# Optimization experiments

Measured on AMD Instinct MI355X. Metric: run time of the kernel, lower is better.

## Reference

```python
import jax, jax.numpy as jnp
import numpy as np
import math

L, N, D = 1024, 64, 64
O = 1024

def setup_inputs() -> dict:
    key = jax.random.key(0)
    k1, k2 = jax.random.split(key)
    x = jax.random.normal(k1, (L, N, D), dtype=jnp.float32)
    upfold = jax.random.normal(k2, (O, N, D), dtype=jnp.float32)
    return {"x": x, "upfold": upfold}

def reference(x, upfold):
    # x: [L, N, D], upfold: [O, N, D]
    d = x.shape[-1]
    scale = 1.0 / math.sqrt(d)
    # affinities: [L, O, N]
    affinities = jnp.einsum('lnd,ond->lon', x, upfold) * scale
    # weighted sum with (sigmoid - 0.5) weights: [L, N, D]
    features = jnp.einsum('lon,ond->lnd', jax.nn.sigmoid(affinities) - 0.5, upfold)
    return features
```

## Files before the change

### kernel.cpp

```cpp
#include <hip/hip_runtime.h>
#include <stdint.h>

#define L_DIM 1024
#define N_DIM 64
#define D_DIM 64
#define O_DIM 1024
#define ND    4096
#define NT    8

typedef float    floatx16 __attribute__((ext_vector_type(16)));
typedef _Float16 half8    __attribute__((ext_vector_type(8)));
typedef _Float16 h2       __attribute__((ext_vector_type(2)));
typedef __fp16   fp16x2   __attribute__((ext_vector_type(2)));

__device__ __forceinline__ uint32_t pkh2(float a, float b) {
    fp16x2 p = __builtin_amdgcn_cvt_pkrtz(a, b);
    return __builtin_bit_cast(uint32_t, p);
}

__device__ __forceinline__ half8 mk_frag(uint32_t a, uint32_t b, uint32_t c, uint32_t d) {
    union { uint32_t u[4]; half8 v; } U;
    U.u[0] = a; U.u[1] = b; U.u[2] = c; U.u[3] = d;
    return U.v;
}

__device__ __forceinline__ uint32_t psig(float s0, float s1) {
    const h2 HI = {(_Float16)41.6f,        (_Float16)41.6f};
    const h2 LO = {(_Float16)-41.6f,       (_Float16)-41.6f};
    const h2 SC = {(_Float16)0.0625f,      (_Float16)0.0625f};
    const h2 C0 = {(_Float16)0.03099238f,  (_Float16)0.03099238f};
    const h2 C1 = {(_Float16)-0.00842090f, (_Float16)-0.00842090f};
    const h2 C2 = {(_Float16)0.00151845f,  (_Float16)0.00151845f};
    const h2 C3 = {(_Float16)-1.02197e-4f, (_Float16)-1.02197e-4f};
    h2 s = __builtin_bit_cast(h2, pkh2(s0, s1));
    s = __builtin_elementwise_min(s, HI);
    s = __builtin_elementwise_max(s, LO);
    h2 ha = s * SC;
    h2 v  = ha * ha;
    h2 w  = C2 + v * C3;
    w     = C1 + v * w;
    w     = C0 + v * w;
    h2 f  = s * w;
    return __builtin_bit_cast(uint32_t, f);
}

__device__ __forceinline__ void load_tile(const float* ubase, int team, int ot,
                                          int g, int c, float4* va, float4* vb) {
    const float* pr = ubase + (size_t)(team * 512 + ot * 64 + 2 * g) * ND + 4 * c;
    #pragma unroll
    for (int j = 0; j < 4; ++j) {
        va[j] = *(const float4*)(pr + (size_t)(16 * j) * ND);
        vb[j] = *(const float4*)(pr + (size_t)(16 * j) * ND + ND);
    }
}

__global__ void __launch_bounds__(256, 4)
corr_kernel(const float* __restrict__ x, const float* __restrict__ up,
            float* __restrict__ out)
{
    __shared__ __align__(16) unsigned char smem[36864];
    uint16_t (*Ub)[64][72]  = (uint16_t (*)[64][72])smem;
    uint32_t (*Ut2)[32][68] = (uint32_t (*)[32][68])(smem + 18432);
    float    (*Fred)[2][2][32][16] = (float (*)[2][2][32][16])smem;
    float    (*Xs)[68] = (float (*)[68])smem;

    const int tid  = threadIdx.x;
    const int lane = tid & 63;
    const int wid  = tid >> 6;
    const int l31  = lane & 31;
    const int h    = lane >> 5;
    const int team = wid >> 1;
    const int wrow = wid & 1;
    const int ttid = tid & 127;
    const int c    = ttid & 15;
    const int g    = ttid >> 4;
    const int n    = blockIdx.x;
    const int lb   = blockIdx.y;
    const int lw   = lb * 64 + wrow * 32 + l31;

    const float* ubase = up + (size_t)n * D_DIM;

    float4 va[4], vb[4];
    load_tile(ubase, team, 0, g, c, va, vb);

    half8 Xf[4];
    {
        const int xr = tid >> 2;
        const int xc = tid & 3;
        const float* xsrc = x + (size_t)(lb * 64 + xr) * ND + n * D_DIM;
        #pragma unroll
        for (int j = 0; j < 4; ++j) {
            float4 f = *(const float4*)(xsrc + 4 * (xc + 4 * j));
            *(float4*)&Xs[xr][4 * (xc + 4 * j)] = f;
        }
        __syncthreads();
        const int rl = wrow * 32 + l31;
        #pragma unroll
        for (int kk = 0; kk < 4; ++kk) {
            float4 f1 = *(const float4*)&Xs[rl][16 * kk + 8 * h];
            float4 f2 = *(const float4*)&Xs[rl][16 * kk + 8 * h + 4];
            Xf[kk] = mk_frag(pkh2(f1.x, f1.y), pkh2(f1.z, f1.w),
                             pkh2(f2.x, f2.y), pkh2(f2.z, f2.w));
        }
        __syncthreads();
    }

    floatx16 F0, F1;
    #pragma unroll
    for (int i = 0; i < 16; ++i) { F0[i] = 0.0f; F1[i] = 0.0f; }

    for (int ot = 0; ot < NT; ++ot) {
        #pragma unroll
        for (int j = 0; j < 4; ++j) {
            uint2 ea = make_uint2(pkh2(va[j].x, va[j].y), pkh2(va[j].z, va[j].w));
            uint2 eb = make_uint2(pkh2(vb[j].x, vb[j].y), pkh2(vb[j].z, vb[j].w));
            *(uint2*)&Ub[team][2*g + 16*j][4*c]     = ea;
            *(uint2*)&Ub[team][2*g + 16*j + 1][4*c] = eb;
            uint4 et = make_uint4(pkh2(va[j].x, vb[j].x), pkh2(va[j].y, vb[j].y),
                                  pkh2(va[j].z, vb[j].z), pkh2(va[j].w, vb[j].w));
            *(uint4*)&Ut2[team][g + 8*j][4*c] = et;
        }
        __syncthreads();

        if (ot + 1 < NT)
            load_tile(ubase, team, ot + 1, g, c, va, vb);

        floatx16 S0, S1;
        #pragma unroll
        for (int i = 0; i < 16; ++i) { S0[i] = 0.0f; S1[i] = 0.0f; }
        #pragma unroll
        for (int kk = 0; kk < 4; ++kk) {
            half8 A0 = *(const half8*)&Ub[team][l31][16 * kk + 8 * h];
            half8 A1 = *(const half8*)&Ub[team][32 + l31][16 * kk + 8 * h];
            S0 = __builtin_amdgcn_mfma_f32_32x32x16_f16(A0, Xf[kk], S0, 0, 0, 0);
            S1 = __builtin_amdgcn_mfma_f32_32x32x16_f16(A1, Xf[kk], S1, 0, 0, 0);
        }

        uint32_t P[16];
        #pragma unroll
        for (int m = 0; m < 8; ++m) P[m]     = psig(S0[2*m], S0[2*m+1]);
        #pragma unroll
        for (int m = 0; m < 8; ++m) P[8 + m] = psig(S1[2*m], S1[2*m+1]);

        uint32_t R[8];
        #pragma unroll
        for (int c2 = 0; c2 < 4; ++c2) {
            const uint32_t* Q = P + (c2 >> 1) * 8;
            const int t4 = (c2 & 1) * 4;
            R[2*c2]   = __shfl_xor(h ? Q[t4]     : Q[t4 + 2], 32);
            R[2*c2+1] = __shfl_xor(h ? Q[t4 + 1] : Q[t4 + 3], 32);
        }
        #pragma unroll
        for (int c2 = 0; c2 < 4; ++c2) {
            const uint32_t* Q = P + (c2 >> 1) * 8;
            const int t4 = (c2 & 1) * 4;
            half8 B = h ? mk_frag(R[2*c2], R[2*c2+1], Q[t4 + 2], Q[t4 + 3])
                        : mk_frag(Q[t4], Q[t4 + 1], R[2*c2], R[2*c2+1]);
            const int opb = 8 * c2 + 4 * h;
            const uint32_t* utp = &Ut2[team][0][0];
            uint32_t a0[4], a1[4];
            #pragma unroll
            for (int k = 0; k < 4; ++k) {
                a0[k] = utp[(opb + k) * 68 + l31];
                a1[k] = utp[(opb + k) * 68 + 32 + l31];
            }
            half8 A0 = mk_frag(a0[0], a0[1], a0[2], a0[3]);
            half8 A1 = mk_frag(a1[0], a1[1], a1[2], a1[3]);
            F0 = __builtin_amdgcn_mfma_f32_32x32x16_f16(A0, B, F0, 0, 0, 0);
            F1 = __builtin_amdgcn_mfma_f32_32x32x16_f16(A1, B, F1, 0, 0, 0);
        }
        __syncthreads();
    }

    {
        float* dst = &Fred[team][wrow][h][l31][0];
        const floatx16& Fexp = team ? F0 : F1;
        #pragma unroll
        for (int q = 0; q < 4; ++q)
            *(float4*)(dst + 4*q) = make_float4(Fexp[4*q], Fexp[4*q+1], Fexp[4*q+2], Fexp[4*q+3]);
    }
    __syncthreads();

    float* op = out + (size_t)lw * ND + n * D_DIM;
    if (team == 0) {
        const float* src = &Fred[1][wrow][h][l31][0];
        #pragma unroll
        for (int q = 0; q < 4; ++q) {
            float4 r = *(const float4*)(src + 4*q);
            float4 a; a.x = F0[4*q]   + r.x; a.y = F0[4*q+1] + r.y;
                      a.z = F0[4*q+2] + r.z; a.w = F0[4*q+3] + r.w;
            *(float4*)(op + 8*q + 4*h) = a;
        }
    } else {
        const float* src = &Fred[0][wrow][h][l31][0];
        #pragma unroll
        for (int q = 0; q < 4; ++q) {
            float4 r = *(const float4*)(src + 4*q);
            float4 a; a.x = F1[4*q]   + r.x; a.y = F1[4*q+1] + r.y;
                      a.z = F1[4*q+2] + r.z; a.w = F1[4*q+3] + r.w;
            *(float4*)(op + 32 + 8*q + 4*h) = a;
        }
    }
}

extern "C" void kernel_launch(void* const* d_in, const int* in_sizes, int n_in,
                              void* d_out, int out_size, void* d_ws, size_t ws_size,
                              hipStream_t stream)
{
    const float* x  = (const float*)d_in[0];
    const float* up = (const float*)d_in[1];
    float* out      = (float*)d_out;
    dim3 grid(N_DIM, L_DIM / 64);
    corr_kernel<<<grid, dim3(256), 0, stream>>>(x, up, out);
}
```

Measured before the change: 104.1 us.

## Drop O-split teams, widen L tile to 128, double-buffer upfold tiles

Each block now takes 128 L rows, with each of the 4 waves owning 32 rows. All waves walk the full O range in 16 tiles instead of two teams each covering half of O. This removes the end-of-kernel LDS cross-team reduction and halves the redundant upfold loads per L row. Upfold tiles are double-buffered in LDS so the next tile is written while the current one is used, with fragments preloaded into registers before the write. The cost is half as many blocks (512), a lower occupancy target of 2 blocks per SM, and a longer serial O loop per wave.

Measured after the change: 101.2 us. -2.8%, faster.

```diff
diff --git a/kernel.cpp b/kernel.cpp
--- a/kernel.cpp
+++ b/kernel.cpp
@@ -6,12 +6,14 @@
 #define D_DIM 64
 #define O_DIM 1024
 #define ND    4096
-#define NT    8
+#define NT    16
 
 typedef float    floatx16 __attribute__((ext_vector_type(16)));
 typedef _Float16 half8    __attribute__((ext_vector_type(8)));
 typedef _Float16 h2       __attribute__((ext_vector_type(2)));
 typedef __fp16   fp16x2   __attribute__((ext_vector_type(2)));
+
+#define BUF_STRIDE 17920
 
 __device__ __forceinline__ uint32_t pkh2(float a, float b) {
     fp16x2 p = __builtin_amdgcn_cvt_pkrtz(a, b);
@@ -44,57 +46,51 @@
     return __builtin_bit_cast(uint32_t, f);
 }
 
-__device__ __forceinline__ void load_tile(const float* ubase, int team, int ot,
-                                          int g, int c, float4* va, float4* vb) {
-    const float* pr = ubase + (size_t)(team * 512 + ot * 64 + 2 * g) * ND + 4 * c;
-    #pragma unroll
-    for (int j = 0; j < 4; ++j) {
-        va[j] = *(const float4*)(pr + (size_t)(16 * j) * ND);
-        vb[j] = *(const float4*)(pr + (size_t)(16 * j) * ND + ND);
-    }
-}
-
-__global__ void __launch_bounds__(256, 4)
+__device__ __forceinline__ void load_tile(const float* ubase, int ot,
+                                          int r8, int c, float4* va, float4* vb) {
+    const float* pr = ubase + (size_t)(ot * 64 + 2 * r8) * ND + 4 * c;
+    #pragma unroll
+    for (int j = 0; j < 2; ++j) {
+        va[j] = *(const float4*)(pr + (size_t)(32 * j) * ND);
+        vb[j] = *(const float4*)(pr + (size_t)(32 * j) * ND + ND);
+    }
+}
+
+__global__ void __launch_bounds__(256, 2)
 corr_kernel(const float* __restrict__ x, const float* __restrict__ up,
             float* __restrict__ out)
 {
-    __shared__ __align__(16) unsigned char smem[36864];
-    uint16_t (*Ub)[64][72]  = (uint16_t (*)[64][72])smem;
-    uint32_t (*Ut2)[32][68] = (uint32_t (*)[32][68])(smem + 18432);
-    float    (*Fred)[2][2][32][16] = (float (*)[2][2][32][16])smem;
-    float    (*Xs)[68] = (float (*)[68])smem;
+    __shared__ __align__(16) unsigned char smem[2 * BUF_STRIDE];
 
     const int tid  = threadIdx.x;
     const int lane = tid & 63;
     const int wid  = tid >> 6;
     const int l31  = lane & 31;
     const int h    = lane >> 5;
-    const int team = wid >> 1;
-    const int wrow = wid & 1;
-    const int ttid = tid & 127;
-    const int c    = ttid & 15;
-    const int g    = ttid >> 4;
+    const int r8   = tid >> 4;
+    const int c    = tid & 15;
     const int n    = blockIdx.x;
     const int lb   = blockIdx.y;
-    const int lw   = lb * 64 + wrow * 32 + l31;
+    const int lw   = lb * 128 + wid * 32 + l31;
 
     const float* ubase = up + (size_t)n * D_DIM;
 
-    float4 va[4], vb[4];
-    load_tile(ubase, team, 0, g, c, va, vb);
+    float4 va[2], vb[2];
+    load_tile(ubase, 0, r8, c, va, vb);
 
     half8 Xf[4];
     {
-        const int xr = tid >> 2;
-        const int xc = tid & 3;
-        const float* xsrc = x + (size_t)(lb * 64 + xr) * ND + n * D_DIM;
-        #pragma unroll
-        for (int j = 0; j < 4; ++j) {
-            float4 f = *(const float4*)(xsrc + 4 * (xc + 4 * j));
-            *(float4*)&Xs[xr][4 * (xc + 4 * j)] = f;
+        float (*Xs)[68] = (float (*)[68])smem;
+        const int xr = tid >> 1;
+        const int xh = tid & 1;
+        const float* xsrc = x + (size_t)(lb * 128 + xr) * ND + n * D_DIM;
+        #pragma unroll
+        for (int j = 0; j < 8; ++j) {
+            const int f4i = xh * 8 + j;
+            *(float4*)&Xs[xr][4 * f4i] = *(const float4*)(xsrc + 4 * f4i);
         }
         __syncthreads();
-        const int rl = wrow * 32 + l31;
+        const int rl = wid * 32 + l31;
         #pragma unroll
         for (int kk = 0; kk < 4; ++kk) {
             float4 f1 = *(const float4*)&Xs[rl][16 * kk + 8 * h];
@@ -105,35 +101,61 @@
         __syncthreads();
     }
 
+    #pragma unroll
+    for (int j = 0; j < 2; ++j) {
+        uint16_t (*Ub)[72]  = (uint16_t (*)[72])(smem);
+        uint32_t (*Ut2)[68] = (uint32_t (*)[68])(smem + 9216);
+        *(uint2*)&Ub[2*r8 + 32*j][4*c] =
+            make_uint2(pkh2(va[j].x, va[j].y), pkh2(va[j].z, va[j].w));
+        *(uint2*)&Ub[2*r8 + 32*j + 1][4*c] =
+            make_uint2(pkh2(vb[j].x, vb[j].y), pkh2(vb[j].z, vb[j].w));
+        *(uint4*)&Ut2[r8 + 16*j][4*c] =
+            make_uint4(pkh2(va[j].x, vb[j].x), pkh2(va[j].y, vb[j].y),
+                       pkh2(va[j].z, vb[j].z), pkh2(va[j].w, vb[j].w));
+    }
+    load_tile(ubase, 1, r8, c, va, vb);
+    __syncthreads();
+
     floatx16 F0, F1;
     #pragma unroll
     for (int i = 0; i < 16; ++i) { F0[i] = 0.0f; F1[i] = 0.0f; }
 
     for (int ot = 0; ot < NT; ++ot) {
-        #pragma unroll
-        for (int j = 0; j < 4; ++j) {
-            uint2 ea = make_uint2(pkh2(va[j].x, va[j].y), pkh2(va[j].z, va[j].w));
-            uint2 eb = make_uint2(pkh2(vb[j].x, vb[j].y), pkh2(vb[j].z, vb[j].w));
-            *(uint2*)&Ub[team][2*g + 16*j][4*c]     = ea;
-            *(uint2*)&Ub[team][2*g + 16*j + 1][4*c] = eb;
-            uint4 et = make_uint4(pkh2(va[j].x, vb[j].x), pkh2(va[j].y, vb[j].y),
-                                  pkh2(va[j].z, vb[j].z), pkh2(va[j].w, vb[j].w));
-            *(uint4*)&Ut2[team][g + 8*j][4*c] = et;
-        }
-        __syncthreads();
-
-        if (ot + 1 < NT)
-            load_tile(ubase, team, ot + 1, g, c, va, vb);
+        const int b = ot & 1;
+        uint16_t (*Ub)[72]   = (uint16_t (*)[72])(smem + b * BUF_STRIDE);
+        const uint32_t* utp  = (const uint32_t*)(smem + b * BUF_STRIDE + 9216);
+        uint16_t (*Ubn)[72]  = (uint16_t (*)[72])(smem + (b ^ 1) * BUF_STRIDE);
+        uint32_t (*Ut2n)[68] = (uint32_t (*)[68])(smem + (b ^ 1) * BUF_STRIDE + 9216);
+
+        half8 A0k[4], A1k[4];
+        #pragma unroll
+        for (int kk = 0; kk < 4; ++kk) {
+            A0k[kk] = *(const half8*)&Ub[l31][16 * kk + 8 * h];
+            A1k[kk] = *(const half8*)&Ub[32 + l31][16 * kk + 8 * h];
+        }
+
+        if (ot + 1 < NT) {
+            #pragma unroll
+            for (int j = 0; j < 2; ++j) {
+                *(uint2*)&Ubn[2*r8 + 32*j][4*c] =
+                    make_uint2(pkh2(va[j].x, va[j].y), pkh2(va[j].z, va[j].w));
+                *(uint2*)&Ubn[2*r8 + 32*j + 1][4*c] =
+                    make_uint2(pkh2(vb[j].x, vb[j].y), pkh2(vb[j].z, vb[j].w));
+                *(uint4*)&Ut2n[r8 + 16*j][4*c] =
+                    make_uint4(pkh2(va[j].x, vb[j].x), pkh2(va[j].y, vb[j].y),
+                               pkh2(va[j].z, vb[j].z), pkh2(va[j].w, vb[j].w));
+            }
+        }
+        if (ot + 2 < NT)
+            load_tile(ubase, ot + 2, r8, c, va, vb);
 
         floatx16 S0, S1;
         #pragma unroll
         for (int i = 0; i < 16; ++i) { S0[i] = 0.0f; S1[i] = 0.0f; }
         #pragma unroll
         for (int kk = 0; kk < 4; ++kk) {
-            half8 A0 = *(const half8*)&Ub[team][l31][16 * kk + 8 * h];
-            half8 A1 = *(const half8*)&Ub[team][32 + l31][16 * kk + 8 * h];
-            S0 = __builtin_amdgcn_mfma_f32_32x32x16_f16(A0, Xf[kk], S0, 0, 0, 0);
-            S1 = __builtin_amdgcn_mfma_f32_32x32x16_f16(A1, Xf[kk], S1, 0, 0, 0);
+            S0 = __builtin_amdgcn_mfma_f32_32x32x16_f16(A0k[kk], Xf[kk], S0, 0, 0, 0);
+            S1 = __builtin_amdgcn_mfma_f32_32x32x16_f16(A1k[kk], Xf[kk], S1, 0, 0, 0);
         }
 
         uint32_t P[16];
@@ -157,7 +179,6 @@
             half8 B = h ? mk_frag(R[2*c2], R[2*c2+1], Q[t4 + 2], Q[t4 + 3])
                         : mk_frag(Q[t4], Q[t4 + 1], R[2*c2], R[2*c2+1]);
             const int opb = 8 * c2 + 4 * h;
-            const uint32_t* utp = &Ut2[team][0][0];
             uint32_t a0[4], a1[4];
             #pragma unroll
             for (int k = 0; k < 4; ++k) {
@@ -172,34 +193,13 @@
         __syncthreads();
     }
 
-    {
-        float* dst = &Fred[team][wrow][h][l31][0];
-        const floatx16& Fexp = team ? F0 : F1;
-        #pragma unroll
-        for (int q = 0; q < 4; ++q)
-            *(float4*)(dst + 4*q) = make_float4(Fexp[4*q], Fexp[4*q+1], Fexp[4*q+2], Fexp[4*q+3]);
-    }
-    __syncthreads();
-
     float* op = out + (size_t)lw * ND + n * D_DIM;
-    if (team == 0) {
-        const float* src = &Fred[1][wrow][h][l31][0];
-        #pragma unroll
-        for (int q = 0; q < 4; ++q) {
-            float4 r = *(const float4*)(src + 4*q);
-            float4 a; a.x = F0[4*q]   + r.x; a.y = F0[4*q+1] + r.y;
-                      a.z = F0[4*q+2] + r.z; a.w = F0[4*q+3] + r.w;
-            *(float4*)(op + 8*q + 4*h) = a;
-        }
-    } else {
-        const float* src = &Fred[0][wrow][h][l31][0];
-        #pragma unroll
-        for (int q = 0; q < 4; ++q) {
-            float4 r = *(const float4*)(src + 4*q);
-            float4 a; a.x = F1[4*q]   + r.x; a.y = F1[4*q+1] + r.y;
-                      a.z = F1[4*q+2] + r.z; a.w = F1[4*q+3] + r.w;
-            *(float4*)(op + 32 + 8*q + 4*h) = a;
-        }
+    #pragma unroll
+    for (int q = 0; q < 4; ++q) {
+        float4 a; a.x = F0[4*q]; a.y = F0[4*q+1]; a.z = F0[4*q+2]; a.w = F0[4*q+3];
+        *(float4*)(op + 8*q + 4*h) = a;
+        float4 bq; bq.x = F1[4*q]; bq.y = F1[4*q+1]; bq.z = F1[4*q+2]; bq.w = F1[4*q+3];
+        *(float4*)(op + 32 + 8*q + 4*h) = bq;
     }
 }
 
@@ -210,6 +210,6 @@
     const float* x  = (const float*)d_in[0];
     const float* up = (const float*)d_in[1];
     float* out      = (float*)d_out;
-    dim3 grid(N_DIM, L_DIM / 64);
+    dim3 grid(N_DIM, L_DIM / 128);
     corr_kernel<<<grid, dim3(256), 0, stream>>>(x, up, out);
 }
```
